# Kernel optimization log

Measured on AMD Instinct MI355X. Metric: run time of the kernel, lower is better.

The kernel has to match this reference:

```python
import jax, jax.numpy as jnp
import numpy as np

N, C_IN, C_HID, C_OUT = 50000, 256, 64 * 4, 64
E = 1_600_000
P_DROP = 0.5


def setup_inputs() -> dict:
    key = jax.random.key(0)
    ks = jax.random.split(key, 12)
    cat = C_IN + C_HID  # DConv input is concat([X, H]) -> in+hidden channels
    glorot = lambda k, sh: jax.random.normal(k, sh, jnp.float32) * (2.0 / (sh[-2] + sh[-1])) ** 0.5
    inp = {
        "x": jax.random.normal(ks[0], (N, C_IN), jnp.float32),
        "edge_index": jax.random.randint(ks[1], (2, E), 0, N, jnp.int64),
        "edge_weight": jax.random.uniform(ks[2], (E,), jnp.float32),
        # deterministic dropout mask (training-mode dropout, p=0.5), pre-scaled by 1/(1-p)
        "mask": (jax.random.uniform(ks[3], (N, C_IN)) >= P_DROP).astype(jnp.float32) / (1.0 - P_DROP),
        # DConv weights: shape (2, K=1, in+hidden, hidden) per gate
        "w_z": glorot(ks[4], (2, 1, cat, C_HID)),
        "b_z": jnp.zeros((C_HID,), jnp.float32),
        "w_r": glorot(ks[5], (2, 1, cat, C_HID)),
        "b_r": jnp.zeros((C_HID,), jnp.float32),
        "w_h": glorot(ks[6], (2, 1, cat, C_HID)),
        "b_h": jnp.zeros((C_HID,), jnp.float32),
        "w_lin": glorot(ks[7], (C_OUT, C_HID)),
        "b_lin": jnp.zeros((C_OUT,), jnp.float32),
    }
    return inp


def _dconv(inp, w, b):
    # K=1 diffusion conv: only the zeroth-order (identity) term of both the
    # forward- and backward-transition expansions survives; edges are unused.
    return inp @ w[0, 0] + inp @ w[1, 0] + b


def reference(x, edge_index, edge_weight, mask, w_z, b_z, w_r, b_r, w_h, b_h, w_lin, b_lin):
    x = x * mask  # F.dropout, training=True, deterministic mask
    H = jnp.zeros((x.shape[0], w_z.shape[-1]), x.dtype)  # initial hidden state
    xh = jnp.concatenate([x, H], axis=1)                  # [N, in+hid]
    Z = jax.nn.sigmoid(_dconv(xh, w_z, b_z))              # update gate
    R = jax.nn.sigmoid(_dconv(xh, w_r, b_r))              # reset gate
    xhr = jnp.concatenate([x, H * R], axis=1)
    H_tilde = jnp.tanh(_dconv(xhr, w_h, b_h))             # candidate state
    H = Z * H + (1.0 - Z) * H_tilde                       # GRU blend
    h = jax.nn.elu(H)
    return h @ w_lin.T + b_lin                            # [N, out]
```

## Files before the change

### kernel.cpp

```cpp
#include <hip/hip_runtime.h>
#include <hip/hip_bf16.h>


typedef __attribute__((ext_vector_type(8))) short bf16x8;
typedef __attribute__((ext_vector_type(4))) float f32x4;

constexpr int N_ROWS = 50000;
constexpr int CIN  = 256;
constexpr int COUT = 64;
constexpr int BM   = 32;

__device__ inline unsigned short f2bf(float f) {
    union { float f; unsigned u; } v; v.f = f;
    unsigned r = v.u + 0x7fffu + ((v.u >> 16) & 1u);
    return (unsigned short)(r >> 16);
}
__device__ inline float bf2f(unsigned short b) {
    union { unsigned u; float f; } v; v.u = ((unsigned)b) << 16;
    return v.f;
}
__device__ inline f32x4 mfma16(bf16x8 a, bf16x8 b, f32x4 c) {
    return __builtin_amdgcn_mfma_f32_16x16x32_bf16(a, b, c, 0, 0, 0);
}

__global__ __launch_bounds__(256) void prep_frags(
    const float* __restrict__ wz, const float* __restrict__ wh,
    const float* __restrict__ wlin, unsigned short* __restrict__ ws)
{
    int t = blockIdx.x * 256 + threadIdx.x;
    int frag = t >> 6, lane = t & 63;
    if (frag >= 288) return;
    int g16 = lane & 15, kg = lane >> 4;
    unsigned short vals[8];
    if (frag < 256) {
        int kb = frag & 7, nf = (frag >> 3) & 15, g = frag >> 7;
        const float* wsrc = g ? wh : wz;
        int n = nf * 16 + g16;
        #pragma unroll
        for (int j = 0; j < 8; ++j) {
            int k = kb * 32 + kg * 8 + j;
            float v = wsrc[k * 256 + n] + wsrc[131072 + k * 256 + n];
            vals[j] = f2bf(v);
        }
    } else {
        int f = frag - 256;
        int kb = f & 7, nf = f >> 3;
        int n = nf * 16 + g16;
        #pragma unroll
        for (int j = 0; j < 8; ++j) {
            int k = kb * 32 + kg * 8 + j;
            vals[j] = f2bf(wlin[n * 256 + k]);
        }
    }
    unsigned short* dst = ws + (size_t)frag * 512 + lane * 8;
    #pragma unroll
    for (int j = 0; j < 8; ++j) dst[j] = vals[j];
}

__device__ inline bf16x8 ldfrag(const unsigned short* wf, int frag, int lane) {
    return *reinterpret_cast<const bf16x8*>(wf + (size_t)frag * 512 + lane * 8);
}

__global__ __launch_bounds__(512, 4) void dcrnn_mfma(
    const float* __restrict__ x, const float* __restrict__ mask,
    const unsigned short* __restrict__ wf,
    const float* __restrict__ bz, const float* __restrict__ bh,
    const float* __restrict__ blin, float* __restrict__ out)
{
    __shared__ char smem[32768];
    char* AhiB = smem;
    char* AloB = smem + 16384;
    const int tid = threadIdx.x, lane = tid & 63, wv = tid >> 6;
    const int l16 = lane & 15, lk = lane >> 4;
    const int row0 = blockIdx.x * BM;
    const int nf0 = wv * 2;

    bf16x8 rZ[2], rH[2];
    rZ[0] = ldfrag(wf, (nf0 + 0)      * 8, lane);
    rH[0] = ldfrag(wf, (16 + nf0 + 0) * 8, lane);
    rZ[1] = ldfrag(wf, (nf0 + 1)      * 8, lane);
    rH[1] = ldfrag(wf, (16 + nf0 + 1) * 8, lane);

    #pragma unroll
    for (int it = 0; it < 4; ++it) {
        int f = it * 512 + tid;
        int r = f >> 6, c4 = f & 63;
        int row = row0 + r;
        float4 xv = make_float4(0.f, 0.f, 0.f, 0.f), mv = xv;
        if (row < N_ROWS) {
            xv = reinterpret_cast<const float4*>(x    + (size_t)row * CIN)[c4];
            mv = reinterpret_cast<const float4*>(mask + (size_t)row * CIN)[c4];
        }
        float v0 = xv.x * mv.x, v1 = xv.y * mv.y, v2 = xv.z * mv.z, v3 = xv.w * mv.w;
        unsigned short h0 = f2bf(v0), h1 = f2bf(v1), h2 = f2bf(v2), h3 = f2bf(v3);
        unsigned short l0 = f2bf(v0 - bf2f(h0)), l1 = f2bf(v1 - bf2f(h1));
        unsigned short l2 = f2bf(v2 - bf2f(h2)), l3 = f2bf(v3 - bf2f(h3));
        int byte = ((r * CIN + c4 * 4) * 2) ^ ((r & 7) << 4);
        *reinterpret_cast<ushort4*>(AhiB + byte) = make_ushort4(h0, h1, h2, h3);
        *reinterpret_cast<ushort4*>(AloB + byte) = make_ushort4(l0, l1, l2, l3);
    }
    __syncthreads();

    f32x4 accZ[2][2], accH[2][2];
    #pragma unroll
    for (int nfi = 0; nfi < 2; ++nfi)
        #pragma unroll
        for (int m = 0; m < 2; ++m) {
            accZ[nfi][m] = (f32x4){0.f, 0.f, 0.f, 0.f};
            accH[nfi][m] = (f32x4){0.f, 0.f, 0.f, 0.f};
        }

    for (int kb = 0; kb < 8; ++kb) {
        bf16x8 ah[2], al[2];
        int koff = kb * 32 + lk * 8;
        #pragma unroll
        for (int m = 0; m < 2; ++m) {
            int row = m * 16 + l16;
            int byte = ((row * CIN + koff) * 2) ^ ((row & 7) << 4);
            ah[m] = *reinterpret_cast<const bf16x8*>(AhiB + byte);
            al[m] = *reinterpret_cast<const bf16x8*>(AloB + byte);
        }
        #pragma unroll
        for (int nfi = 0; nfi < 2; ++nfi) {
            int nkb = kb < 7 ? kb + 1 : 7;
            bf16x8 nZ = ldfrag(wf, (nf0 + nfi)      * 8 + nkb, lane);
            bf16x8 nH = ldfrag(wf, (16 + nf0 + nfi) * 8 + nkb, lane);
            #pragma unroll
            for (int m = 0; m < 2; ++m) {
                accZ[nfi][m] = mfma16(ah[m], rZ[nfi], accZ[nfi][m]);
                accZ[nfi][m] = mfma16(al[m], rZ[nfi], accZ[nfi][m]);
                accH[nfi][m] = mfma16(ah[m], rH[nfi], accH[nfi][m]);
                accH[nfi][m] = mfma16(al[m], rH[nfi], accH[nfi][m]);
            }
            rZ[nfi] = nZ; rH[nfi] = nH;
        }
    }

    bf16x8 cb = ldfrag(wf, 256 + (wv & 3) * 8, lane);

    __syncthreads();

    #pragma unroll
    for (int nfi = 0; nfi < 2; ++nfi) {
        int col = wv * 32 + nfi * 16 + l16;
        float bzv = bz[col], bhv = bh[col];
        #pragma unroll
        for (int m = 0; m < 2; ++m) {
            #pragma unroll
            for (int i = 0; i < 4; ++i) {
                float z  = 1.f / (1.f + __expf(-(accZ[nfi][m][i] + bzv)));
                float t  = __expf(2.f * (accH[nfi][m][i] + bhv));
                float th = (t - 1.f) / (t + 1.f);
                float H  = (1.f - z) * th;
                float h  = (H > 0.f) ? H : (__expf(H) - 1.f);
                int row = m * 16 + lk * 4 + i;
                unsigned pk = ((unsigned)f2bf(h)) << 16;
                int byte = (row * 1024 + col * 4) ^ ((row & 7) << 4);
                *reinterpret_cast<unsigned*>(smem + byte) = pk;
            }
        }
    }
    __syncthreads();

    f32x4 accO = (f32x4){0.f, 0.f, 0.f, 0.f};
    const int mo = wv >> 2;
    for (int kb = 0; kb < 8; ++kb) {
        int nk = kb < 7 ? kb + 1 : 7;
        bf16x8 nb = ldfrag(wf, 256 + (wv & 3) * 8 + nk, lane);
        int row = mo * 16 + l16;
        int e0  = kb * 32 + lk * 8;
        int b0  = (row * 1024 + e0 * 4)      ^ ((row & 7) << 4);
        int b1  = (row * 1024 + e0 * 4 + 16) ^ ((row & 7) << 4);
        uint4 p0 = *reinterpret_cast<const uint4*>(smem + b0);
        uint4 p1 = *reinterpret_cast<const uint4*>(smem + b1);
        bf16x8 ha;
        ha[0] = (short)(p0.x >> 16); ha[1] = (short)(p0.y >> 16);
        ha[2] = (short)(p0.z >> 16); ha[3] = (short)(p0.w >> 16);
        ha[4] = (short)(p1.x >> 16); ha[5] = (short)(p1.y >> 16);
        ha[6] = (short)(p1.z >> 16); ha[7] = (short)(p1.w >> 16);
        accO = mfma16(ha, cb, accO);
        cb = nb;
    }
    {
        int col = (wv & 3) * 16 + l16;
        float bo = blin[col];
        #pragma unroll
        for (int i = 0; i < 4; ++i) {
            int row = row0 + mo * 16 + lk * 4 + i;
            if (row < N_ROWS) out[(size_t)row * COUT + col] = accO[i] + bo;
        }
    }
}

__global__ __launch_bounds__(256) void fallback_f32(
    const float* __restrict__ x, const float* __restrict__ mask,
    const float* __restrict__ wzr, const float* __restrict__ whr,
    const float* __restrict__ bz, const float* __restrict__ bh,
    const float* __restrict__ wlinr, const float* __restrict__ blin,
    float* __restrict__ out)
{
    __shared__ float xm[32][CIN];
    const int tid = threadIdx.x;
    const int row0 = blockIdx.x * 32;
    #pragma unroll
    for (int it = 0; it < 8; ++it) {
        int idx = it * 256 + tid;
        int r = idx >> 6, c4 = idx & 63, row = row0 + r;
        float4 v = make_float4(0.f, 0.f, 0.f, 0.f);
        if (row < N_ROWS) {
            float4 a = reinterpret_cast<const float4*>(x    + (size_t)row * CIN)[c4];
            float4 m = reinterpret_cast<const float4*>(mask + (size_t)row * CIN)[c4];
            v = make_float4(a.x * m.x, a.y * m.y, a.z * m.z, a.w * m.w);
        }
        reinterpret_cast<float4*>(&xm[r][0])[c4] = v;
    }
    __syncthreads();
    const int j0 = (tid & 63) * 4, r0 = (tid >> 6) * 8;
    float accz[4][8], acch[4][8];
    #pragma unroll
    for (int c = 0; c < 4; ++c)
        #pragma unroll
        for (int r = 0; r < 8; ++r) { accz[c][r] = 0.f; acch[c][r] = 0.f; }
    for (int k = 0; k < CIN; k += 4) {
        float4 wz4[4], wh4[4];
        #pragma unroll
        for (int kk = 0; kk < 4; ++kk) {
            float4 a0 = *reinterpret_cast<const float4*>(&wzr[(k + kk) * 256 + j0]);
            float4 a1 = *reinterpret_cast<const float4*>(&wzr[131072 + (k + kk) * 256 + j0]);
            wz4[kk] = make_float4(a0.x + a1.x, a0.y + a1.y, a0.z + a1.z, a0.w + a1.w);
            float4 b0 = *reinterpret_cast<const float4*>(&whr[(k + kk) * 256 + j0]);
            float4 b1 = *reinterpret_cast<const float4*>(&whr[131072 + (k + kk) * 256 + j0]);
            wh4[kk] = make_float4(b0.x + b1.x, b0.y + b1.y, b0.z + b1.z, b0.w + b1.w);
        }
        #pragma unroll
        for (int r = 0; r < 8; ++r) {
            float4 xv = *reinterpret_cast<const float4*>(&xm[r0 + r][k]);
            float xk[4] = {xv.x, xv.y, xv.z, xv.w};
            float wzc[4][4] = {{wz4[0].x,wz4[0].y,wz4[0].z,wz4[0].w},{wz4[1].x,wz4[1].y,wz4[1].z,wz4[1].w},
                               {wz4[2].x,wz4[2].y,wz4[2].z,wz4[2].w},{wz4[3].x,wz4[3].y,wz4[3].z,wz4[3].w}};
            float whc[4][4] = {{wh4[0].x,wh4[0].y,wh4[0].z,wh4[0].w},{wh4[1].x,wh4[1].y,wh4[1].z,wh4[1].w},
                               {wh4[2].x,wh4[2].y,wh4[2].z,wh4[2].w},{wh4[3].x,wh4[3].y,wh4[3].z,wh4[3].w}};
            #pragma unroll
            for (int kk = 0; kk < 4; ++kk)
                #pragma unroll
                for (int c = 0; c < 4; ++c) {
                    accz[c][r] = fmaf(xk[kk], wzc[kk][c], accz[c][r]);
                    acch[c][r] = fmaf(xk[kk], whc[kk][c], acch[c][r]);
                }
        }
    }
    float bzj[4], bhj[4];
    #pragma unroll
    for (int c = 0; c < 4; ++c) { bzj[c] = bz[j0 + c]; bhj[c] = bh[j0 + c]; }
    __syncthreads();
    #pragma unroll
    for (int r = 0; r < 8; ++r) {
        float hc[4];
        #pragma unroll
        for (int c = 0; c < 4; ++c) {
            float z  = 1.f / (1.f + expf(-(accz[c][r] + bzj[c])));
            float ht = tanhf(acch[c][r] + bhj[c]);
            float H  = (1.f - z) * ht;
            hc[c] = (H > 0.f) ? H : expm1f(H);
        }
        *reinterpret_cast<float4*>(&xm[r0 + r][j0]) = make_float4(hc[0], hc[1], hc[2], hc[3]);
    }
    __syncthreads();
    const int o = tid & 63;
    float acc[8];
    #pragma unroll
    for (int r = 0; r < 8; ++r) acc[r] = 0.f;
    for (int k = 0; k < CIN; k += 4) {
        float4 wv4 = *reinterpret_cast<const float4*>(&wlinr[o * 256 + k]);
        #pragma unroll
        for (int r = 0; r < 8; ++r) {
            float4 hv = *reinterpret_cast<const float4*>(&xm[r0 + r][k]);
            acc[r] = fmaf(hv.x, wv4.x, acc[r]);
            acc[r] = fmaf(hv.y, wv4.y, acc[r]);
            acc[r] = fmaf(hv.z, wv4.z, acc[r]);
            acc[r] = fmaf(hv.w, wv4.w, acc[r]);
        }
    }
    float bo = blin[o];
    #pragma unroll
    for (int r = 0; r < 8; ++r) {
        int row = row0 + r0 + r;
        if (row < N_ROWS) out[(size_t)row * COUT + o] = acc[r] + bo;
    }
}

extern "C" void kernel_launch(void* const* d_in, const int* in_sizes, int n_in,
                              void* d_out, int out_size, void* d_ws, size_t ws_size,
                              hipStream_t stream)
{
    const float* x    = (const float*)d_in[0];
    const float* mask = (const float*)d_in[3];
    const float* wz   = (const float*)d_in[4];
    const float* bz   = (const float*)d_in[5];
    const float* wh   = (const float*)d_in[8];
    const float* bh   = (const float*)d_in[9];
    const float* wlin = (const float*)d_in[10];
    const float* blin = (const float*)d_in[11];
    float* outf = (float*)d_out;

    const size_t ws_need = 288 * 1024;
    if (ws_size >= ws_need) {
        unsigned short* wsf = (unsigned short*)d_ws;
        prep_frags<<<72, 256, 0, stream>>>(wz, wh, wlin, wsf);
        dcrnn_mfma<<<(N_ROWS + BM - 1) / BM, 512, 0, stream>>>(
            x, mask, wsf, bz, bh, blin, outf);
    } else {
        fallback_f32<<<(N_ROWS + 31) / 32, 256, 0, stream>>>(
            x, mask, wz, wh, bz, bh, wlin, blin, outf);
    }
}
```

Before: 62.69 us.

## Make fused DCRNN kernel persistent with register-resident weights and prefetched tiles

Replaces the one-block-per-tile launch with a persistent grid of 512 blocks that loop over row tiles. Each block loads its Z/H weight fragments into registers and the output-layer weights into LDS once, instead of reloading them for every tile. Inside the loop it prefetches the next tile's x and mask into registers while the current tile is processed. The cost is higher register pressure (launch bounds drop to 2 blocks per CU), more LDS per block, and an extra barrier per tile, so there may be less latency hiding from occupancy.

```diff
diff --git a/kernel.cpp b/kernel.cpp
--- a/kernel.cpp
+++ b/kernel.cpp
@@ -9,6 +9,8 @@
 constexpr int CIN  = 256;
 constexpr int COUT = 64;
 constexpr int BM   = 32;
+constexpr int NTILES = (N_ROWS + BM - 1) / BM;
+constexpr int GRID = 512;
 
 __device__ inline unsigned short f2bf(float f) {
     union { float f; unsigned u; } v; v.f = f;
@@ -61,134 +63,163 @@
     return *reinterpret_cast<const bf16x8*>(wf + (size_t)frag * 512 + lane * 8);
 }
 
-__global__ __launch_bounds__(512, 4) void dcrnn_mfma(
+__global__ __launch_bounds__(512, 2) void dcrnn_persist(
     const float* __restrict__ x, const float* __restrict__ mask,
     const unsigned short* __restrict__ wf,
     const float* __restrict__ bz, const float* __restrict__ bh,
     const float* __restrict__ blin, float* __restrict__ out)
 {
-    __shared__ char smem[32768];
+    __shared__ char smem[65536];
     char* AhiB = smem;
     char* AloB = smem + 16384;
+    unsigned short* owLDS = reinterpret_cast<unsigned short*>(smem + 32768);
+
     const int tid = threadIdx.x, lane = tid & 63, wv = tid >> 6;
     const int l16 = lane & 15, lk = lane >> 4;
-    const int row0 = blockIdx.x * BM;
     const int nf0 = wv * 2;
 
-    bf16x8 rZ[2], rH[2];
-    rZ[0] = ldfrag(wf, (nf0 + 0)      * 8, lane);
-    rH[0] = ldfrag(wf, (16 + nf0 + 0) * 8, lane);
-    rZ[1] = ldfrag(wf, (nf0 + 1)      * 8, lane);
-    rH[1] = ldfrag(wf, (16 + nf0 + 1) * 8, lane);
-
-    #pragma unroll
-    for (int it = 0; it < 4; ++it) {
-        int f = it * 512 + tid;
-        int r = f >> 6, c4 = f & 63;
-        int row = row0 + r;
-        float4 xv = make_float4(0.f, 0.f, 0.f, 0.f), mv = xv;
-        if (row < N_ROWS) {
-            xv = reinterpret_cast<const float4*>(x    + (size_t)row * CIN)[c4];
-            mv = reinterpret_cast<const float4*>(mask + (size_t)row * CIN)[c4];
-        }
-        float v0 = xv.x * mv.x, v1 = xv.y * mv.y, v2 = xv.z * mv.z, v3 = xv.w * mv.w;
-        unsigned short h0 = f2bf(v0), h1 = f2bf(v1), h2 = f2bf(v2), h3 = f2bf(v3);
-        unsigned short l0 = f2bf(v0 - bf2f(h0)), l1 = f2bf(v1 - bf2f(h1));
-        unsigned short l2 = f2bf(v2 - bf2f(h2)), l3 = f2bf(v3 - bf2f(h3));
-        int byte = ((r * CIN + c4 * 4) * 2) ^ ((r & 7) << 4);
-        *reinterpret_cast<ushort4*>(AhiB + byte) = make_ushort4(h0, h1, h2, h3);
-        *reinterpret_cast<ushort4*>(AloB + byte) = make_ushort4(l0, l1, l2, l3);
-    }
-    __syncthreads();
-
-    f32x4 accZ[2][2], accH[2][2];
+    bf16x8 wZ[2][8], wH[2][8];
     #pragma unroll
     for (int nfi = 0; nfi < 2; ++nfi)
         #pragma unroll
-        for (int m = 0; m < 2; ++m) {
-            accZ[nfi][m] = (f32x4){0.f, 0.f, 0.f, 0.f};
-            accH[nfi][m] = (f32x4){0.f, 0.f, 0.f, 0.f};
-        }
-
-    for (int kb = 0; kb < 8; ++kb) {
-        bf16x8 ah[2], al[2];
-        int koff = kb * 32 + lk * 8;
-        #pragma unroll
-        for (int m = 0; m < 2; ++m) {
-            int row = m * 16 + l16;
-            int byte = ((row * CIN + koff) * 2) ^ ((row & 7) << 4);
-            ah[m] = *reinterpret_cast<const bf16x8*>(AhiB + byte);
-            al[m] = *reinterpret_cast<const bf16x8*>(AloB + byte);
-        }
-        #pragma unroll
-        for (int nfi = 0; nfi < 2; ++nfi) {
-            int nkb = kb < 7 ? kb + 1 : 7;
-            bf16x8 nZ = ldfrag(wf, (nf0 + nfi)      * 8 + nkb, lane);
-            bf16x8 nH = ldfrag(wf, (16 + nf0 + nfi) * 8 + nkb, lane);
-            #pragma unroll
-            for (int m = 0; m < 2; ++m) {
-                accZ[nfi][m] = mfma16(ah[m], rZ[nfi], accZ[nfi][m]);
-                accZ[nfi][m] = mfma16(al[m], rZ[nfi], accZ[nfi][m]);
-                accH[nfi][m] = mfma16(ah[m], rH[nfi], accH[nfi][m]);
-                accH[nfi][m] = mfma16(al[m], rH[nfi], accH[nfi][m]);
-            }
-            rZ[nfi] = nZ; rH[nfi] = nH;
-        }
-    }
-
-    bf16x8 cb = ldfrag(wf, 256 + (wv & 3) * 8, lane);
-
-    __syncthreads();
-
+        for (int kb = 0; kb < 8; ++kb) {
+            wZ[nfi][kb] = ldfrag(wf, (nf0 + nfi) * 8 + kb, lane);
+            wH[nfi][kb] = ldfrag(wf, (16 + nf0 + nfi) * 8 + kb, lane);
+        }
+    {
+        const uint4* src = reinterpret_cast<const uint4*>(wf + 256 * 512);
+        uint4* dst = reinterpret_cast<uint4*>(owLDS);
+        #pragma unroll
+        for (int i = 0; i < 4; ++i) dst[i * 512 + tid] = src[i * 512 + tid];
+    }
+    float bzv[2], bhv[2];
     #pragma unroll
     for (int nfi = 0; nfi < 2; ++nfi) {
         int col = wv * 32 + nfi * 16 + l16;
-        float bzv = bz[col], bhv = bh[col];
-        #pragma unroll
-        for (int m = 0; m < 2; ++m) {
-            #pragma unroll
-            for (int i = 0; i < 4; ++i) {
-                float z  = 1.f / (1.f + __expf(-(accZ[nfi][m][i] + bzv)));
-                float t  = __expf(2.f * (accH[nfi][m][i] + bhv));
-                float th = (t - 1.f) / (t + 1.f);
-                float H  = (1.f - z) * th;
-                float h  = (H > 0.f) ? H : (__expf(H) - 1.f);
-                int row = m * 16 + lk * 4 + i;
-                unsigned pk = ((unsigned)f2bf(h)) << 16;
-                int byte = (row * 1024 + col * 4) ^ ((row & 7) << 4);
-                *reinterpret_cast<unsigned*>(smem + byte) = pk;
+        bzv[nfi] = bz[col]; bhv[nfi] = bh[col];
+    }
+    const int ocol = (wv & 3) * 16 + l16;
+    const float bo = blin[ocol];
+    const int mo = wv >> 2;
+
+    int t = blockIdx.x;
+    float4 px[4], pm[4];
+    #pragma unroll
+    for (int it = 0; it < 4; ++it) {
+        int s = it * 512 + tid, r = s >> 6, c4 = s & 63;
+        int row = t * BM + r;
+        px[it] = make_float4(0.f, 0.f, 0.f, 0.f); pm[it] = px[it];
+        if (row < N_ROWS) {
+            px[it] = reinterpret_cast<const float4*>(x    + (size_t)row * CIN)[c4];
+            pm[it] = reinterpret_cast<const float4*>(mask + (size_t)row * CIN)[c4];
+        }
+    }
+    __syncthreads();
+
+    for (; t < NTILES; t += GRID) {
+        #pragma unroll
+        for (int it = 0; it < 4; ++it) {
+            int s = it * 512 + tid, r = s >> 6, c4 = s & 63;
+            float v0 = px[it].x * pm[it].x, v1 = px[it].y * pm[it].y;
+            float v2 = px[it].z * pm[it].z, v3 = px[it].w * pm[it].w;
+            unsigned short h0 = f2bf(v0), h1 = f2bf(v1), h2 = f2bf(v2), h3 = f2bf(v3);
+            unsigned short l0 = f2bf(v0 - bf2f(h0)), l1 = f2bf(v1 - bf2f(h1));
+            unsigned short l2 = f2bf(v2 - bf2f(h2)), l3 = f2bf(v3 - bf2f(h3));
+            int byte = ((r * CIN + c4 * 4) * 2) ^ ((r & 7) << 4);
+            *reinterpret_cast<ushort4*>(AhiB + byte) = make_ushort4(h0, h1, h2, h3);
+            *reinterpret_cast<ushort4*>(AloB + byte) = make_ushort4(l0, l1, l2, l3);
+        }
+        int tn = t + GRID;
+        if (tn < NTILES) {
+            #pragma unroll
+            for (int it = 0; it < 4; ++it) {
+                int s = it * 512 + tid, r = s >> 6, c4 = s & 63;
+                int row = tn * BM + r;
+                px[it] = make_float4(0.f, 0.f, 0.f, 0.f); pm[it] = px[it];
+                if (row < N_ROWS) {
+                    px[it] = reinterpret_cast<const float4*>(x    + (size_t)row * CIN)[c4];
+                    pm[it] = reinterpret_cast<const float4*>(mask + (size_t)row * CIN)[c4];
+                }
             }
         }
-    }
-    __syncthreads();
-
-    f32x4 accO = (f32x4){0.f, 0.f, 0.f, 0.f};
-    const int mo = wv >> 2;
-    for (int kb = 0; kb < 8; ++kb) {
-        int nk = kb < 7 ? kb + 1 : 7;
-        bf16x8 nb = ldfrag(wf, 256 + (wv & 3) * 8 + nk, lane);
-        int row = mo * 16 + l16;
-        int e0  = kb * 32 + lk * 8;
-        int b0  = (row * 1024 + e0 * 4)      ^ ((row & 7) << 4);
-        int b1  = (row * 1024 + e0 * 4 + 16) ^ ((row & 7) << 4);
-        uint4 p0 = *reinterpret_cast<const uint4*>(smem + b0);
-        uint4 p1 = *reinterpret_cast<const uint4*>(smem + b1);
-        bf16x8 ha;
-        ha[0] = (short)(p0.x >> 16); ha[1] = (short)(p0.y >> 16);
-        ha[2] = (short)(p0.z >> 16); ha[3] = (short)(p0.w >> 16);
-        ha[4] = (short)(p1.x >> 16); ha[5] = (short)(p1.y >> 16);
-        ha[6] = (short)(p1.z >> 16); ha[7] = (short)(p1.w >> 16);
-        accO = mfma16(ha, cb, accO);
-        cb = nb;
-    }
-    {
-        int col = (wv & 3) * 16 + l16;
-        float bo = blin[col];
+        __syncthreads();
+
+        f32x4 accZ[2][2], accH[2][2];
+        #pragma unroll
+        for (int nfi = 0; nfi < 2; ++nfi)
+            #pragma unroll
+            for (int m = 0; m < 2; ++m) {
+                accZ[nfi][m] = (f32x4){0.f, 0.f, 0.f, 0.f};
+                accH[nfi][m] = (f32x4){0.f, 0.f, 0.f, 0.f};
+            }
+        #pragma unroll
+        for (int kb = 0; kb < 8; ++kb) {
+            bf16x8 ah[2], al[2];
+            int koff = kb * 32 + lk * 8;
+            #pragma unroll
+            for (int m = 0; m < 2; ++m) {
+                int row = m * 16 + l16;
+                int byte = ((row * CIN + koff) * 2) ^ ((row & 7) << 4);
+                ah[m] = *reinterpret_cast<const bf16x8*>(AhiB + byte);
+                al[m] = *reinterpret_cast<const bf16x8*>(AloB + byte);
+            }
+            #pragma unroll
+            for (int nfi = 0; nfi < 2; ++nfi)
+                #pragma unroll
+                for (int m = 0; m < 2; ++m) {
+                    accZ[nfi][m] = mfma16(ah[m], wZ[nfi][kb], accZ[nfi][m]);
+                    accZ[nfi][m] = mfma16(al[m], wZ[nfi][kb], accZ[nfi][m]);
+                    accH[nfi][m] = mfma16(ah[m], wH[nfi][kb], accH[nfi][m]);
+                    accH[nfi][m] = mfma16(al[m], wH[nfi][kb], accH[nfi][m]);
+                }
+        }
+        __syncthreads();
+
+        #pragma unroll
+        for (int nfi = 0; nfi < 2; ++nfi) {
+            int col = wv * 32 + nfi * 16 + l16;
+            #pragma unroll
+            for (int m = 0; m < 2; ++m) {
+                #pragma unroll
+                for (int i = 0; i < 4; ++i) {
+                    float z  = 1.f / (1.f + __expf(-(accZ[nfi][m][i] + bzv[nfi])));
+                    float tt = __expf(2.f * (accH[nfi][m][i] + bhv[nfi]));
+                    float th = (tt - 1.f) / (tt + 1.f);
+                    float H  = (1.f - z) * th;
+                    float h  = (H > 0.f) ? H : (__expf(H) - 1.f);
+                    int row = m * 16 + lk * 4 + i;
+                    unsigned pk = ((unsigned)f2bf(h)) << 16;
+                    int byte = (row * 1024 + col * 4) ^ ((row & 7) << 4);
+                    *reinterpret_cast<unsigned*>(smem + byte) = pk;
+                }
+            }
+        }
+        __syncthreads();
+
+        f32x4 accO = (f32x4){0.f, 0.f, 0.f, 0.f};
+        #pragma unroll
+        for (int kb = 0; kb < 8; ++kb) {
+            bf16x8 cb = *reinterpret_cast<const bf16x8*>(
+                owLDS + (size_t)((wv & 3) * 8 + kb) * 512 + lane * 8);
+            int row = mo * 16 + l16;
+            int e0  = kb * 32 + lk * 8;
+            int b0  = (row * 1024 + e0 * 4)      ^ ((row & 7) << 4);
+            int b1  = (row * 1024 + e0 * 4 + 16) ^ ((row & 7) << 4);
+            uint4 p0 = *reinterpret_cast<const uint4*>(smem + b0);
+            uint4 p1 = *reinterpret_cast<const uint4*>(smem + b1);
+            bf16x8 ha;
+            ha[0] = (short)(p0.x >> 16); ha[1] = (short)(p0.y >> 16);
+            ha[2] = (short)(p0.z >> 16); ha[3] = (short)(p0.w >> 16);
+            ha[4] = (short)(p1.x >> 16); ha[5] = (short)(p1.y >> 16);
+            ha[6] = (short)(p1.z >> 16); ha[7] = (short)(p1.w >> 16);
+            accO = mfma16(ha, cb, accO);
+        }
         #pragma unroll
         for (int i = 0; i < 4; ++i) {
-            int row = row0 + mo * 16 + lk * 4 + i;
-            if (row < N_ROWS) out[(size_t)row * COUT + col] = accO[i] + bo;
-        }
+            int row = t * BM + mo * 16 + lk * 4 + i;
+            if (row < N_ROWS) out[(size_t)row * COUT + ocol] = accO[i] + bo;
+        }
+        __syncthreads();
     }
 }
 
@@ -307,7 +338,7 @@
     if (ws_size >= ws_need) {
         unsigned short* wsf = (unsigned short*)d_ws;
         prep_frags<<<72, 256, 0, stream>>>(wz, wh, wlin, wsf);
-        dcrnn_mfma<<<(N_ROWS + BM - 1) / BM, 512, 0, stream>>>(
+        dcrnn_persist<<<GRID, 512, 0, stream>>>(
             x, mask, wsf, bz, bh, blin, outf);
     } else {
         fallback_f32<<<(N_ROWS + 31) / 32, 256, 0, stream>>>(
```

Measured after the change: 106.4 us. 69.6% more time.

## Stage weight fragments through LDS with async global_load_lds pipelining

Applied to the files above, without the earlier changes.

Weight fragments for the gate and output GEMMs are now streamed into a per-wave LDS buffer with global_load_lds, replacing register prefetch. Explicit vmcnt/lgkmcnt waits overlap the next k-block's weight fetch with the current MFMAs. Bias loads are also hoisted ahead of the main loop. Shared memory grows from 32KB to 64KB per block, which may reduce blocks per CU. The hand-placed waitcnt asm is fragile against compiler reordering, and the x/mask global loads in the staging loop also increment vmcnt, which could make the counting wrong.

```diff
diff --git a/kernel.cpp b/kernel.cpp
--- a/kernel.cpp
+++ b/kernel.cpp
@@ -21,6 +21,11 @@
 }
 __device__ inline f32x4 mfma16(bf16x8 a, bf16x8 b, f32x4 c) {
     return __builtin_amdgcn_mfma_f32_16x16x32_bf16(a, b, c, 0, 0, 0);
+}
+__device__ __forceinline__ void gload16(const void* g, void* l) {
+    __builtin_amdgcn_global_load_lds(
+        (const __attribute__((address_space(1))) char*)g,
+        (__attribute__((address_space(3))) char*)l, 16, 0, 0);
 }
 
 __global__ __launch_bounds__(256) void prep_frags(
@@ -57,34 +62,50 @@
     for (int j = 0; j < 8; ++j) dst[j] = vals[j];
 }
 
-__device__ inline bf16x8 ldfrag(const unsigned short* wf, int frag, int lane) {
-    return *reinterpret_cast<const bf16x8*>(wf + (size_t)frag * 512 + lane * 8);
-}
-
-__global__ __launch_bounds__(512, 4) void dcrnn_mfma(
+__global__ __launch_bounds__(512)
+__attribute__((amdgpu_waves_per_eu(4, 4)))
+void dcrnn_async(
     const float* __restrict__ x, const float* __restrict__ mask,
     const unsigned short* __restrict__ wf,
     const float* __restrict__ bz, const float* __restrict__ bh,
     const float* __restrict__ blin, float* __restrict__ out)
 {
-    __shared__ char smem[32768];
+    __shared__ char smem[65536];
     char* AhiB = smem;
     char* AloB = smem + 16384;
     const int tid = threadIdx.x, lane = tid & 63, wv = tid >> 6;
     const int l16 = lane & 15, lk = lane >> 4;
     const int row0 = blockIdx.x * BM;
     const int nf0 = wv * 2;
-
-    bf16x8 rZ[2], rH[2];
-    rZ[0] = ldfrag(wf, (nf0 + 0)      * 8, lane);
-    rH[0] = ldfrag(wf, (16 + nf0 + 0) * 8, lane);
-    rZ[1] = ldfrag(wf, (nf0 + 1)      * 8, lane);
-    rH[1] = ldfrag(wf, (16 + nf0 + 1) * 8, lane);
+    char* wbuf = smem + 32768 + wv * 4096;
+
+    auto stage_gate = [&](int kb, int g) {
+        char* dst = wbuf + g * 2048;
+        gload16(wf + (size_t)((g * 16 + nf0)     * 8 + kb) * 512 + lane * 8, dst);
+        gload16(wf + (size_t)((g * 16 + nf0 + 1) * 8 + kb) * 512 + lane * 8, dst + 1024);
+    };
+    auto stage_out = [&](int v) {
+        char* dst = wbuf + (v & 1) * 2048;
+        gload16(wf + (size_t)(256 + (wv & 3) * 8 + 2 * v)     * 512 + lane * 8, dst);
+        gload16(wf + (size_t)(256 + (wv & 3) * 8 + 2 * v + 1) * 512 + lane * 8, dst + 1024);
+    };
+
+    stage_gate(0, 0);
+    stage_gate(0, 1);
+
+    float bzv[2], bhv[2];
+    #pragma unroll
+    for (int nfi = 0; nfi < 2; ++nfi) {
+        int col = wv * 32 + nfi * 16 + l16;
+        bzv[nfi] = bz[col]; bhv[nfi] = bh[col];
+    }
+    const int ocol = (wv & 3) * 16 + l16;
+    const float bo = blin[ocol];
+    const int mo = wv >> 2;
 
     #pragma unroll
     for (int it = 0; it < 4; ++it) {
-        int f = it * 512 + tid;
-        int r = f >> 6, c4 = f & 63;
+        int s = it * 512 + tid, r = s >> 6, c4 = s & 63;
         int row = row0 + r;
         float4 xv = make_float4(0.f, 0.f, 0.f, 0.f), mv = xv;
         if (row < N_ROWS) {
@@ -120,37 +141,43 @@
             ah[m] = *reinterpret_cast<const bf16x8*>(AhiB + byte);
             al[m] = *reinterpret_cast<const bf16x8*>(AloB + byte);
         }
-        #pragma unroll
-        for (int nfi = 0; nfi < 2; ++nfi) {
-            int nkb = kb < 7 ? kb + 1 : 7;
-            bf16x8 nZ = ldfrag(wf, (nf0 + nfi)      * 8 + nkb, lane);
-            bf16x8 nH = ldfrag(wf, (16 + nf0 + nfi) * 8 + nkb, lane);
-            #pragma unroll
-            for (int m = 0; m < 2; ++m) {
-                accZ[nfi][m] = mfma16(ah[m], rZ[nfi], accZ[nfi][m]);
-                accZ[nfi][m] = mfma16(al[m], rZ[nfi], accZ[nfi][m]);
-                accH[nfi][m] = mfma16(ah[m], rH[nfi], accH[nfi][m]);
-                accH[nfi][m] = mfma16(al[m], rH[nfi], accH[nfi][m]);
-            }
-            rZ[nfi] = nZ; rH[nfi] = nH;
-        }
-    }
-
-    bf16x8 cb = ldfrag(wf, 256 + (wv & 3) * 8, lane);
-
+        if (kb >= 1) asm volatile("s_waitcnt vmcnt(2)" ::: "memory");
+        bf16x8 zb0 = *reinterpret_cast<const bf16x8*>(wbuf + lane * 16);
+        bf16x8 zb1 = *reinterpret_cast<const bf16x8*>(wbuf + 1024 + lane * 16);
+        asm volatile("s_waitcnt lgkmcnt(0)" ::: "memory");
+        if (kb < 7) stage_gate(kb + 1, 0); else stage_out(0);
+        #pragma unroll
+        for (int m = 0; m < 2; ++m) {
+            accZ[0][m] = mfma16(ah[m], zb0, accZ[0][m]);
+            accZ[0][m] = mfma16(al[m], zb0, accZ[0][m]);
+            accZ[1][m] = mfma16(ah[m], zb1, accZ[1][m]);
+            accZ[1][m] = mfma16(al[m], zb1, accZ[1][m]);
+        }
+        if (kb >= 1) asm volatile("s_waitcnt vmcnt(2)" ::: "memory");
+        bf16x8 hb0 = *reinterpret_cast<const bf16x8*>(wbuf + 2048 + lane * 16);
+        bf16x8 hb1 = *reinterpret_cast<const bf16x8*>(wbuf + 3072 + lane * 16);
+        asm volatile("s_waitcnt lgkmcnt(0)" ::: "memory");
+        if (kb < 7) stage_gate(kb + 1, 1); else stage_out(1);
+        #pragma unroll
+        for (int m = 0; m < 2; ++m) {
+            accH[0][m] = mfma16(ah[m], hb0, accH[0][m]);
+            accH[0][m] = mfma16(al[m], hb0, accH[0][m]);
+            accH[1][m] = mfma16(ah[m], hb1, accH[1][m]);
+            accH[1][m] = mfma16(al[m], hb1, accH[1][m]);
+        }
+    }
     __syncthreads();
 
     #pragma unroll
     for (int nfi = 0; nfi < 2; ++nfi) {
         int col = wv * 32 + nfi * 16 + l16;
-        float bzv = bz[col], bhv = bh[col];
         #pragma unroll
         for (int m = 0; m < 2; ++m) {
             #pragma unroll
             for (int i = 0; i < 4; ++i) {
-                float z  = 1.f / (1.f + __expf(-(accZ[nfi][m][i] + bzv)));
-                float t  = __expf(2.f * (accH[nfi][m][i] + bhv));
-                float th = (t - 1.f) / (t + 1.f);
+                float z  = 1.f / (1.f + __expf(-(accZ[nfi][m][i] + bzv[nfi])));
+                float tt = __expf(2.f * (accH[nfi][m][i] + bhv[nfi]));
+                float th = (tt - 1.f) / (tt + 1.f);
                 float H  = (1.f - z) * th;
                 float h  = (H > 0.f) ? H : (__expf(H) - 1.f);
                 int row = m * 16 + lk * 4 + i;
@@ -163,32 +190,34 @@
     __syncthreads();
 
     f32x4 accO = (f32x4){0.f, 0.f, 0.f, 0.f};
-    const int mo = wv >> 2;
-    for (int kb = 0; kb < 8; ++kb) {
-        int nk = kb < 7 ? kb + 1 : 7;
-        bf16x8 nb = ldfrag(wf, 256 + (wv & 3) * 8 + nk, lane);
-        int row = mo * 16 + l16;
-        int e0  = kb * 32 + lk * 8;
-        int b0  = (row * 1024 + e0 * 4)      ^ ((row & 7) << 4);
-        int b1  = (row * 1024 + e0 * 4 + 16) ^ ((row & 7) << 4);
-        uint4 p0 = *reinterpret_cast<const uint4*>(smem + b0);
-        uint4 p1 = *reinterpret_cast<const uint4*>(smem + b1);
-        bf16x8 ha;
-        ha[0] = (short)(p0.x >> 16); ha[1] = (short)(p0.y >> 16);
-        ha[2] = (short)(p0.z >> 16); ha[3] = (short)(p0.w >> 16);
-        ha[4] = (short)(p1.x >> 16); ha[5] = (short)(p1.y >> 16);
-        ha[6] = (short)(p1.z >> 16); ha[7] = (short)(p1.w >> 16);
-        accO = mfma16(ha, cb, accO);
-        cb = nb;
-    }
-    {
-        int col = (wv & 3) * 16 + l16;
-        float bo = blin[col];
-        #pragma unroll
-        for (int i = 0; i < 4; ++i) {
-            int row = row0 + mo * 16 + lk * 4 + i;
-            if (row < N_ROWS) out[(size_t)row * COUT + col] = accO[i] + bo;
-        }
+    for (int v = 0; v < 4; ++v) {
+        if (v == 2) asm volatile("s_waitcnt vmcnt(2)" ::: "memory");
+        if (v == 3) asm volatile("s_waitcnt vmcnt(0)" ::: "memory");
+        bf16x8 cb0 = *reinterpret_cast<const bf16x8*>(wbuf + (v & 1) * 2048 + lane * 16);
+        bf16x8 cb1 = *reinterpret_cast<const bf16x8*>(wbuf + (v & 1) * 2048 + 1024 + lane * 16);
+        asm volatile("s_waitcnt lgkmcnt(0)" ::: "memory");
+        if (v < 2) stage_out(v + 2);
+        #pragma unroll
+        for (int j = 0; j < 2; ++j) {
+            int kb = 2 * v + j;
+            int row = mo * 16 + l16;
+            int e0  = kb * 32 + lk * 8;
+            int b0  = (row * 1024 + e0 * 4)      ^ ((row & 7) << 4);
+            int b1  = (row * 1024 + e0 * 4 + 16) ^ ((row & 7) << 4);
+            uint4 p0 = *reinterpret_cast<const uint4*>(smem + b0);
+            uint4 p1 = *reinterpret_cast<const uint4*>(smem + b1);
+            bf16x8 ha;
+            ha[0] = (short)(p0.x >> 16); ha[1] = (short)(p0.y >> 16);
+            ha[2] = (short)(p0.z >> 16); ha[3] = (short)(p0.w >> 16);
+            ha[4] = (short)(p1.x >> 16); ha[5] = (short)(p1.y >> 16);
+            ha[6] = (short)(p1.z >> 16); ha[7] = (short)(p1.w >> 16);
+            accO = mfma16(ha, j ? cb1 : cb0, accO);
+        }
+    }
+    #pragma unroll
+    for (int i = 0; i < 4; ++i) {
+        int row = row0 + mo * 16 + lk * 4 + i;
+        if (row < N_ROWS) out[(size_t)row * COUT + ocol] = accO[i] + bo;
     }
 }
 
@@ -307,7 +336,7 @@
     if (ws_size >= ws_need) {
         unsigned short* wsf = (unsigned short*)d_ws;
         prep_frags<<<72, 256, 0, stream>>>(wz, wh, wlin, wsf);
-        dcrnn_mfma<<<(N_ROWS + BM - 1) / BM, 512, 0, stream>>>(
+        dcrnn_async<<<(N_ROWS + BM - 1) / BM, 512, 0, stream>>>(
             x, mask, wsf, bz, bh, blin, outf);
     } else {
         fallback_f32<<<(N_ROWS + 31) / 32, 256, 0, stream>>>(
```

Result: no change. 61.68 us (-1.6%).
